# Performance work log

Measured on AMD Instinct MI355X. Metric: run time of the kernel, lower is better.

The kernel has to match this reference:

```python
import jax, jax.numpy as jnp
import numpy as np

BN_EPS = 1e-5


def _sparse(x, idx, W, b):
    # x: [B, N], idx: [N, K] int, W: [N, K], b: [N]
    # out[b, j] = sum_k x[b, idx[j, k]] * W[j, k] + b[j]
    g = jnp.take(x, idx, axis=1)            # [B, N, K]
    return jnp.einsum('bjk,jk->bj', g, W) + b


def _bn_train(x, gamma, beta):
    # BatchNorm1d in training mode: batch stats, biased variance
    m = jnp.mean(x, axis=0)
    v = jnp.mean(jnp.square(x - m), axis=0)
    return gamma * (x - m) * jax.lax.rsqrt(v + BN_EPS) + beta


def setup_inputs() -> dict:
    key = jax.random.key(0)
    ks = jax.random.split(key, 12)
    B, N = 16384, 784
    s = 0.5  # modest weight scale to keep the deep reuse-chain numerically tame
    return {
        'x':    jax.random.normal(ks[0], (B, N), dtype=jnp.float32),
        'idx1': jax.random.randint(ks[1], (N, 2), 0, N, dtype=jnp.int32),
        'W1':   jax.random.normal(ks[2], (N, 2), dtype=jnp.float32) * s,
        'b1':   jax.random.normal(ks[3], (N,), dtype=jnp.float32) * 0.1,
        'idx2': jax.random.randint(ks[4], (N, 4), 0, N, dtype=jnp.int32),
        'W2':   jax.random.normal(ks[5], (N, 4), dtype=jnp.float32) * s,
        'b2':   jax.random.normal(ks[6], (N,), dtype=jnp.float32) * 0.1,
        'idx3': jax.random.randint(ks[7], (N, 8), 0, N, dtype=jnp.int32),
        'W3':   jax.random.normal(ks[8], (N, 8), dtype=jnp.float32) * s,
        'b3':   jax.random.normal(ks[9], (N,), dtype=jnp.float32) * 0.1,
        'g2':   jnp.ones((N,), dtype=jnp.float32),
        'be2':  jnp.zeros((N,), dtype=jnp.float32),
        'g3':   jnp.ones((N,), dtype=jnp.float32),
        'be3':  jnp.zeros((N,), dtype=jnp.float32),
    }


def reference(x, idx1, W1, b1, idx2, W2, b2, idx3, W3, b3, g2, be2, g3, be3):
    gelu = lambda h: jax.nn.gelu(h, approximate=False)  # torch nn.GELU default (exact)
    h = gelu(_sparse(x, idx1, W1, b1))                  # sp1 -> gelu
    h = _bn_train(gelu(_sparse(h, idx2, W2, b2)), g2, be2)   # sp2 -> gelu -> bn2
    h = _bn_train(gelu(_sparse(h, idx3, W3, b3)), g3, be3)   # sp3 -> gelu -> bn3
    h = _bn_train(gelu(_sparse(h, idx2, W2, b2)), g2, be2)   # sp2 (reused) -> gelu -> bn2
    h = jax.nn.relu(_sparse(h, idx1, W1, b1))                # sp1 (reused) -> relu
    return h
```

## Files before the change

kernel.cpp:

```cpp
#include <hip/hip_runtime.h>
#include <math.h>

static constexpr int BROWS   = 16384;
static constexpr int NC      = 784;
static constexpr int TRB     = 16;
static constexpr int THREADS = 256;
static constexpr int NBLK    = BROWS / TRB;
static constexpr int NSLOT   = 4;
static constexpr int NREP    = 4;
static constexpr float EPS   = 1e-5f;
static constexpr float INV_B = 1.0f / (float)BROWS;

#if defined(__has_builtin)
#if __has_builtin(__builtin_amdgcn_global_load_lds)
#define HAVE_ASYNC_LDS 1
#endif
#if __has_builtin(__builtin_amdgcn_rcpf)
#define HAVE_RCPF 1
#endif
#if __has_builtin(__builtin_elementwise_fma)
#define HAVE_EW_FMA 1
#endif
#endif

typedef float v2f __attribute__((ext_vector_type(2)));

__device__ __forceinline__ void stage16(const float4* g, float4* l) {
#ifdef HAVE_ASYNC_LDS
    __builtin_amdgcn_global_load_lds(
        (const __attribute__((address_space(1))) void*)g,
        (__attribute__((address_space(3))) void*)l, 16, 0, 0);
#else
    *l = *g;
#endif
}

__device__ __forceinline__ unsigned short f2b(float f) {
    union { float f; unsigned u; } v; v.f = f;
    const unsigned r = v.u + 0x7fffu + ((v.u >> 16) & 1u);
    return (unsigned short)(r >> 16);
}
__device__ __forceinline__ unsigned pack2(float lo, float hi) {
    return (unsigned)f2b(lo) | ((unsigned)f2b(hi) << 16);
}
__device__ __forceinline__ unsigned long long pack4(float a, float b, float c, float d) {
    return (unsigned long long)pack2(a, b) | ((unsigned long long)pack2(c, d) << 32);
}
__device__ __forceinline__ float fast_rcp(float x) {
#ifdef HAVE_RCPF
    return __builtin_amdgcn_rcpf(x);
#else
    return 1.0f / x;
#endif
}

__device__ __forceinline__ float gelu_f(float x) {
    const float u  = x * x;
    const float z  = x * fmaf(0.0356774081f, u, 0.7978845608f);
    const float e  = __expf(2.0f * z);
    const float r  = fast_rcp(e + 1.0f);
    const float t  = fmaf(-2.0f, r, 1.0f);
    const float hx = 0.5f * x;
    return fmaf(hx, t, hx);
}

__device__ __forceinline__ void fmaq(const unsigned long long v, const float w, v2f acc[2]) {
    const unsigned lo = (unsigned)v, hi = (unsigned)(v >> 32);
    union { unsigned u; float f; } a0, a1, b0, b1;
    a0.u = lo << 16; a1.u = lo & 0xffff0000u;
    b0.u = hi << 16; b1.u = hi & 0xffff0000u;
    const v2f a = { a0.f, a1.f }, b = { b0.f, b1.f };
    const v2f w2 = { w, w };
#ifdef HAVE_EW_FMA
    acc[0] = __builtin_elementwise_fma(a, w2, acc[0]);
    acc[1] = __builtin_elementwise_fma(b, w2, acc[1]);
#else
    acc[0] += a * w2;
    acc[1] += b * w2;
#endif
}

template<int CH>
__device__ __forceinline__ void gchunk(const unsigned long long* __restrict__ tile,
                                       const int* ji, const float* jw,
                                       v2f acc[4][2])
{
    unsigned long long t[CH][4];
    #pragma unroll
    for (int k = 0; k < CH; ++k) {
        #pragma unroll
        for (int q = 0; q < 4; ++q) t[k][q] = tile[q * NC + ji[k]];
    }
    #pragma unroll
    for (int k = 0; k < CH; ++k) {
        #pragma unroll
        for (int q = 0; q < 4; ++q) fmaq(t[k][q], jw[k], acc[q]);
    }
}

template<int K>
__device__ __forceinline__ void gacc(const unsigned long long* __restrict__ tile,
                                     const int* ji, const float* jw, const float jb,
                                     v2f acc[4][2])
{
    #pragma unroll
    for (int q = 0; q < 4; ++q) { acc[q][0] = (v2f){ jb, jb }; acc[q][1] = (v2f){ jb, jb }; }
    if (K == 8) {
        gchunk<4>(tile, ji,     jw,     acc);
        gchunk<4>(tile, ji + 4, jw + 4, acc);
    } else {
        gchunk<K>(tile, ji, jw, acc);
    }
}

__global__ __launch_bounds__(THREADS, 5)
void k12(const float* __restrict__ x,
         const int* __restrict__ idx1, const float* __restrict__ W1, const float* __restrict__ b1,
         const int* __restrict__ idx2, const float* __restrict__ W2, const float* __restrict__ b2,
         unsigned long long* __restrict__ outr,
         float* __restrict__ ssum, float* __restrict__ ssq)
{
    __shared__ unsigned long long tile[4 * NC];
    const int tid  = threadIdx.x;
    const int row0 = blockIdx.x * TRB;

    #pragma unroll
    for (int s = 0; s < NSLOT; ++s) {
        const int c = tid + s * THREADS;
        if (c < NC) {
            #pragma unroll
            for (int q = 0; q < 4; ++q) {
                const size_t base = (size_t)(row0 + 4 * q) * NC + c;
                tile[q * NC + c] = pack4(x[base], x[base + NC], x[base + 2 * NC], x[base + 3 * NC]);
            }
        }
    }
    __syncthreads();

    unsigned long long o[NSLOT][4];
    #pragma unroll
    for (int s = 0; s < NSLOT; ++s) {
        const int j = tid + s * THREADS;
        if (j < NC) {
            int ji[2]; float jw[2];
            ji[0] = idx1[2 * j]; ji[1] = idx1[2 * j + 1];
            jw[0] = W1[2 * j];   jw[1] = W1[2 * j + 1];
            v2f acc[4][2];
            gacc<2>(tile, ji, jw, b1[j], acc);
            #pragma unroll
            for (int q = 0; q < 4; ++q)
                o[s][q] = pack4(gelu_f(acc[q][0].x), gelu_f(acc[q][0].y),
                                gelu_f(acc[q][1].x), gelu_f(acc[q][1].y));
        }
    }
    __syncthreads();
    #pragma unroll
    for (int s = 0; s < NSLOT; ++s) {
        const int j = tid + s * THREADS;
        if (j < NC) {
            #pragma unroll
            for (int q = 0; q < 4; ++q) tile[q * NC + j] = o[s][q];
        }
    }
    __syncthreads();

    const int rep = blockIdx.x & (NREP - 1);
    unsigned long long* dst = outr + (size_t)blockIdx.x * 4 * NC;
    #pragma unroll
    for (int s = 0; s < NSLOT; ++s) {
        const int j = tid + s * THREADS;
        if (j < NC) {
            int ji[4]; float jw[4];
            #pragma unroll
            for (int k = 0; k < 4; ++k) { ji[k] = idx2[4 * j + k]; jw[k] = W2[4 * j + k]; }
            v2f acc[4][2];
            gacc<4>(tile, ji, jw, b2[j], acc);
            float s1 = 0.0f, s2 = 0.0f;
            #pragma unroll
            for (int q = 0; q < 4; ++q) {
                const float u0 = gelu_f(acc[q][0].x), u1 = gelu_f(acc[q][0].y);
                const float u2 = gelu_f(acc[q][1].x), u3 = gelu_f(acc[q][1].y);
                s1 += (u0 + u1) + (u2 + u3);
                s2 = fmaf(u0, u0, fmaf(u1, u1, fmaf(u2, u2, fmaf(u3, u3, s2))));
                dst[q * NC + j] = pack4(u0, u1, u2, u3);
            }
            atomicAdd(&ssum[rep * NC + j], s1);
            atomicAdd(&ssq[rep * NC + j],  s2);
        }
    }
}

template<int K, bool FINAL>
__global__ __launch_bounds__(THREADS, 5)
void kbn(const unsigned long long* __restrict__ inr,
         const int* __restrict__ idx, const float* __restrict__ W, const float* __restrict__ bias,
         const float* __restrict__ gamma, const float* __restrict__ beta,
         const float* __restrict__ psum, const float* __restrict__ psq,
         unsigned long long* __restrict__ outr, float* __restrict__ fout,
         float* __restrict__ ssum, float* __restrict__ ssq)
{
    __shared__ unsigned long long tile[4 * NC];
    __shared__ float s_sc[NC], s_sh[NC];
    const int tid  = threadIdx.x;
    const int row0 = blockIdx.x * TRB;

    {
        const float4* src = (const float4*)(inr + (size_t)blockIdx.x * 4 * NC);
        float4*       dstl = (float4*)tile;
        for (int i = tid; i < 4 * NC / 2; i += THREADS) stage16(src + i, dstl + i);
    }
    for (int j = tid; j < NC; j += THREADS) {
        float s1 = 0.0f, s2 = 0.0f;
        #pragma unroll
        for (int r = 0; r < NREP; ++r) { s1 += psum[r * NC + j]; s2 += psq[r * NC + j]; }
        const float m   = s1 * INV_B;
        const float var = fmaf(-m, m, s2 * INV_B);
        const float sc  = gamma[j] * rsqrtf(var + EPS);
        s_sc[j] = sc;
        s_sh[j] = fmaf(-m, sc, beta[j]);
    }
    __syncthreads();

    const int rep = blockIdx.x & (NREP - 1);
    unsigned long long* dst = FINAL ? nullptr : (outr + (size_t)blockIdx.x * 4 * NC);
    #pragma unroll
    for (int s = 0; s < NSLOT; ++s) {
        const int j = tid + s * THREADS;
        if (j < NC) {
            int ji[K]; float jw[K];
            float jb = bias[j];
            #pragma unroll
            for (int k = 0; k < K; ++k) {
                const int   c = idx[K * j + k];
                const float w = W[K * j + k];
                ji[k] = c; jw[k] = w * s_sc[c]; jb = fmaf(w, s_sh[c], jb);
            }
            v2f acc[4][2];
            gacc<K>(tile, ji, jw, jb, acc);
            if (FINAL) {
                #pragma unroll
                for (int q = 0; q < 4; ++q) {
                    fout[(size_t)(row0 + 4 * q + 0) * NC + j] = fmaxf(acc[q][0].x, 0.0f);
                    fout[(size_t)(row0 + 4 * q + 1) * NC + j] = fmaxf(acc[q][0].y, 0.0f);
                    fout[(size_t)(row0 + 4 * q + 2) * NC + j] = fmaxf(acc[q][1].x, 0.0f);
                    fout[(size_t)(row0 + 4 * q + 3) * NC + j] = fmaxf(acc[q][1].y, 0.0f);
                }
            } else {
                float s1 = 0.0f, s2 = 0.0f;
                #pragma unroll
                for (int q = 0; q < 4; ++q) {
                    const float u0 = gelu_f(acc[q][0].x), u1 = gelu_f(acc[q][0].y);
                    const float u2 = gelu_f(acc[q][1].x), u3 = gelu_f(acc[q][1].y);
                    s1 += (u0 + u1) + (u2 + u3);
                    s2 = fmaf(u0, u0, fmaf(u1, u1, fmaf(u2, u2, fmaf(u3, u3, s2))));
                    dst[q * NC + j] = pack4(u0, u1, u2, u3);
                }
                atomicAdd(&ssum[rep * NC + j], s1);
                atomicAdd(&ssq[rep * NC + j],  s2);
            }
        }
    }
}

extern "C" void kernel_launch(void* const* d_in, const int* in_sizes, int n_in,
                              void* d_out, int out_size, void* d_ws, size_t ws_size,
                              hipStream_t stream)
{
    const float* x    = (const float*)d_in[0];
    const int*   idx1 = (const int*)  d_in[1];
    const float* W1   = (const float*)d_in[2];
    const float* b1   = (const float*)d_in[3];
    const int*   idx2 = (const int*)  d_in[4];
    const float* W2   = (const float*)d_in[5];
    const float* b2   = (const float*)d_in[6];
    const int*   idx3 = (const int*)  d_in[7];
    const float* W3   = (const float*)d_in[8];
    const float* b3   = (const float*)d_in[9];
    const float* g2   = (const float*)d_in[10];
    const float* be2  = (const float*)d_in[11];
    const float* g3   = (const float*)d_in[12];
    const float* be3  = (const float*)d_in[13];
    float* out = (float*)d_out;

    const size_t QN = (size_t)NBLK * 4 * NC;
    unsigned long long* r0 = (unsigned long long*)d_ws;
    unsigned long long* r1 = r0 + QN;
    float* p = (float*)(r1 + QN);
    float* sum2a = p; p += NREP * NC;  float* ssq2a = p; p += NREP * NC;
    float* sum3  = p; p += NREP * NC;  float* ssq3  = p; p += NREP * NC;
    float* sum2b = p; p += NREP * NC;  float* ssq2b = p; p += NREP * NC;

    hipMemsetAsync(sum2a, 0, 6 * NREP * NC * sizeof(float), stream);

    const dim3 grid(NBLK), blk(THREADS);

    k12<<<grid, blk, 0, stream>>>(x, idx1, W1, b1, idx2, W2, b2, r0, sum2a, ssq2a);
    kbn<8, false><<<grid, blk, 0, stream>>>(
        r0, idx3, W3, b3, g2, be2, sum2a, ssq2a, r1, nullptr, sum3, ssq3);
    kbn<4, false><<<grid, blk, 0, stream>>>(
        r1, idx2, W2, b2, g3, be3, sum3, ssq3, r0, nullptr, sum2b, ssq2b);
    kbn<2, true><<<grid, blk, 0, stream>>>(
        r0, idx1, W1, b1, g2, be2, sum2b, ssq2b, nullptr, out, nullptr, nullptr);
}
```

Measured before the change: 197.6 us.

## Fuse all sparse layers into one cooperative persistent kernel with grid barriers

Adds a cooperative kernel that keeps each block's 16-row tile in LDS across all five sparse layers. At each BatchNorm boundary it synchronises the whole grid with an arrive counter: the last block to arrive reduces the batch statistics and publishes the scale and shift, and the other blocks spin on a flag. This removes the bf16 intermediate round trips through global memory and three extra kernel launches. In exchange it needs every block resident at once, at 4 blocks per CU, and adds three grid-wide barriers, each with one block doing the reduction alone. The fallback multi-kernel path is retuned to 512 threads with split LDS tiles.

New measurement: 628.6 us. +218.1%, slower.

```diff
diff --git a/kernel.cpp b/kernel.cpp
--- a/kernel.cpp
+++ b/kernel.cpp
@@ -4,12 +4,15 @@
 static constexpr int BROWS   = 16384;
 static constexpr int NC      = 784;
 static constexpr int TRB     = 16;
-static constexpr int THREADS = 256;
 static constexpr int NBLK    = BROWS / TRB;
-static constexpr int NSLOT   = 4;
 static constexpr int NREP    = 4;
 static constexpr float EPS   = 1e-5f;
 static constexpr float INV_B = 1.0f / (float)BROWS;
+
+static constexpr int PTHREADS = 256;
+static constexpr int PNSLOT   = 4;
+static constexpr int FTHREADS = 512;
+static constexpr int FNSLOT   = 2;
 
 #if defined(__has_builtin)
 #if __has_builtin(__builtin_amdgcn_global_load_lds)
@@ -45,6 +48,12 @@
 }
 __device__ __forceinline__ unsigned long long pack4(float a, float b, float c, float d) {
     return (unsigned long long)pack2(a, b) | ((unsigned long long)pack2(c, d) << 32);
+}
+__device__ __forceinline__ unsigned long long pack_f2(float a, float b) {
+    union { float f[2]; unsigned long long u; } v; v.f[0] = a; v.f[1] = b; return v.u;
+}
+__device__ __forceinline__ void unpack_f2(unsigned long long u, float& a, float& b) {
+    union { float f[2]; unsigned long long u; } v; v.u = u; a = v.f[0]; b = v.f[1];
 }
 __device__ __forceinline__ float fast_rcp(float x) {
 #ifdef HAVE_RCPF
@@ -113,119 +122,22 @@
     }
 }
 
-__global__ __launch_bounds__(THREADS, 5)
-void k12(const float* __restrict__ x,
-         const int* __restrict__ idx1, const float* __restrict__ W1, const float* __restrict__ b1,
-         const int* __restrict__ idx2, const float* __restrict__ W2, const float* __restrict__ b2,
-         unsigned long long* __restrict__ outr,
-         float* __restrict__ ssum, float* __restrict__ ssq)
-{
-    __shared__ unsigned long long tile[4 * NC];
-    const int tid  = threadIdx.x;
-    const int row0 = blockIdx.x * TRB;
-
-    #pragma unroll
-    for (int s = 0; s < NSLOT; ++s) {
-        const int c = tid + s * THREADS;
-        if (c < NC) {
-            #pragma unroll
-            for (int q = 0; q < 4; ++q) {
-                const size_t base = (size_t)(row0 + 4 * q) * NC + c;
-                tile[q * NC + c] = pack4(x[base], x[base + NC], x[base + 2 * NC], x[base + 3 * NC]);
-            }
-        }
-    }
-    __syncthreads();
-
-    unsigned long long o[NSLOT][4];
-    #pragma unroll
-    for (int s = 0; s < NSLOT; ++s) {
-        const int j = tid + s * THREADS;
-        if (j < NC) {
-            int ji[2]; float jw[2];
-            ji[0] = idx1[2 * j]; ji[1] = idx1[2 * j + 1];
-            jw[0] = W1[2 * j];   jw[1] = W1[2 * j + 1];
-            v2f acc[4][2];
-            gacc<2>(tile, ji, jw, b1[j], acc);
-            #pragma unroll
-            for (int q = 0; q < 4; ++q)
-                o[s][q] = pack4(gelu_f(acc[q][0].x), gelu_f(acc[q][0].y),
-                                gelu_f(acc[q][1].x), gelu_f(acc[q][1].y));
-        }
-    }
-    __syncthreads();
-    #pragma unroll
-    for (int s = 0; s < NSLOT; ++s) {
-        const int j = tid + s * THREADS;
-        if (j < NC) {
-            #pragma unroll
-            for (int q = 0; q < 4; ++q) tile[q * NC + j] = o[s][q];
-        }
-    }
-    __syncthreads();
-
-    const int rep = blockIdx.x & (NREP - 1);
-    unsigned long long* dst = outr + (size_t)blockIdx.x * 4 * NC;
-    #pragma unroll
-    for (int s = 0; s < NSLOT; ++s) {
-        const int j = tid + s * THREADS;
-        if (j < NC) {
-            int ji[4]; float jw[4];
-            #pragma unroll
-            for (int k = 0; k < 4; ++k) { ji[k] = idx2[4 * j + k]; jw[k] = W2[4 * j + k]; }
-            v2f acc[4][2];
-            gacc<4>(tile, ji, jw, b2[j], acc);
-            float s1 = 0.0f, s2 = 0.0f;
-            #pragma unroll
-            for (int q = 0; q < 4; ++q) {
-                const float u0 = gelu_f(acc[q][0].x), u1 = gelu_f(acc[q][0].y);
-                const float u2 = gelu_f(acc[q][1].x), u3 = gelu_f(acc[q][1].y);
-                s1 += (u0 + u1) + (u2 + u3);
-                s2 = fmaf(u0, u0, fmaf(u1, u1, fmaf(u2, u2, fmaf(u3, u3, s2))));
-                dst[q * NC + j] = pack4(u0, u1, u2, u3);
-            }
-            atomicAdd(&ssum[rep * NC + j], s1);
-            atomicAdd(&ssq[rep * NC + j],  s2);
-        }
-    }
-}
-
-template<int K, bool FINAL>
-__global__ __launch_bounds__(THREADS, 5)
-void kbn(const unsigned long long* __restrict__ inr,
-         const int* __restrict__ idx, const float* __restrict__ W, const float* __restrict__ bias,
-         const float* __restrict__ gamma, const float* __restrict__ beta,
-         const float* __restrict__ psum, const float* __restrict__ psq,
-         unsigned long long* __restrict__ outr, float* __restrict__ fout,
-         float* __restrict__ ssum, float* __restrict__ ssq)
-{
-    __shared__ unsigned long long tile[4 * NC];
-    __shared__ float s_sc[NC], s_sh[NC];
-    const int tid  = threadIdx.x;
-    const int row0 = blockIdx.x * TRB;
-
-    {
-        const float4* src = (const float4*)(inr + (size_t)blockIdx.x * 4 * NC);
-        float4*       dstl = (float4*)tile;
-        for (int i = tid; i < 4 * NC / 2; i += THREADS) stage16(src + i, dstl + i);
-    }
-    for (int j = tid; j < NC; j += THREADS) {
-        float s1 = 0.0f, s2 = 0.0f;
-        #pragma unroll
-        for (int r = 0; r < NREP; ++r) { s1 += psum[r * NC + j]; s2 += psq[r * NC + j]; }
-        const float m   = s1 * INV_B;
-        const float var = fmaf(-m, m, s2 * INV_B);
-        const float sc  = gamma[j] * rsqrtf(var + EPS);
-        s_sc[j] = sc;
-        s_sh[j] = fmaf(-m, sc, beta[j]);
-    }
-    __syncthreads();
-
-    const int rep = blockIdx.x & (NREP - 1);
-    unsigned long long* dst = FINAL ? nullptr : (outr + (size_t)blockIdx.x * 4 * NC);
-    #pragma unroll
-    for (int s = 0; s < NSLOT; ++s) {
-        const int j = tid + s * THREADS;
+
+template<int K, bool FOLD, bool STATS, bool FINAL>
+__device__ __forceinline__ void pphase(
+    unsigned long long* __restrict__ tile,
+    const float* __restrict__ s_sc, const float* __restrict__ s_sh,
+    const int* __restrict__ idx, const float* __restrict__ W,
+    const float* __restrict__ bias,
+    const int tid, const int row0, const int rep,
+    float* __restrict__ psum, float* __restrict__ psq,
+    float* __restrict__ fout)
+{
+    unsigned long long o[PNSLOT][4];
+    float st1[PNSLOT], st2[PNSLOT];
+    #pragma unroll
+    for (int s = 0; s < PNSLOT; ++s) {
+        const int j = tid + s * PTHREADS;
         if (j < NC) {
             int ji[K]; float jw[K];
             float jb = bias[j];
@@ -233,7 +145,9 @@
             for (int k = 0; k < K; ++k) {
                 const int   c = idx[K * j + k];
                 const float w = W[K * j + k];
-                ji[k] = c; jw[k] = w * s_sc[c]; jb = fmaf(w, s_sh[c], jb);
+                ji[k] = c;
+                if (FOLD) { jw[k] = w * s_sc[c]; jb = fmaf(w, s_sh[c], jb); }
+                else      { jw[k] = w; }
             }
             v2f acc[4][2];
             gacc<K>(tile, ji, jw, jb, acc);
@@ -251,10 +165,273 @@
                 for (int q = 0; q < 4; ++q) {
                     const float u0 = gelu_f(acc[q][0].x), u1 = gelu_f(acc[q][0].y);
                     const float u2 = gelu_f(acc[q][1].x), u3 = gelu_f(acc[q][1].y);
+                    if (STATS) {
+                        s1 += (u0 + u1) + (u2 + u3);
+                        s2 = fmaf(u0, u0, fmaf(u1, u1, fmaf(u2, u2, fmaf(u3, u3, s2))));
+                    }
+                    o[s][q] = pack4(u0, u1, u2, u3);
+                }
+                st1[s] = s1; st2[s] = s2;
+            }
+        }
+    }
+    if (FINAL) return;
+    __syncthreads();
+    #pragma unroll
+    for (int s = 0; s < PNSLOT; ++s) {
+        const int j = tid + s * PTHREADS;
+        if (j < NC) {
+            #pragma unroll
+            for (int q = 0; q < 4; ++q) tile[q * NC + j] = o[s][q];
+            if (STATS) {
+                atomicAdd(&psum[rep * NC + j], st1[s]);
+                atomicAdd(&psq [rep * NC + j], st2[s]);
+            }
+        }
+    }
+    __syncthreads();
+}
+
+__device__ __forceinline__ void bn_barrier(
+    const int tid, const int bno,
+    const float* __restrict__ psum, const float* __restrict__ psq,
+    const float* __restrict__ gamma, const float* __restrict__ beta,
+    unsigned long long* __restrict__ scshG,
+    unsigned* __restrict__ arrive, unsigned* __restrict__ flag,
+    float* __restrict__ s_sc, float* __restrict__ s_sh, int* __restrict__ s_last)
+{
+    if (tid == 0) {
+        __threadfence();
+        const unsigned t = __hip_atomic_fetch_add(&arrive[bno], 1u,
+                              __ATOMIC_ACQ_REL, __HIP_MEMORY_SCOPE_AGENT);
+        *s_last = (t == (unsigned)(NBLK - 1));
+    }
+    __syncthreads();
+    if (*s_last) {
+        for (int j = tid; j < NC; j += PTHREADS) {
+            float s1 = 0.0f, s2 = 0.0f;
+            #pragma unroll
+            for (int r = 0; r < NREP; ++r) {
+                s1 += __hip_atomic_load(&psum[r * NC + j], __ATOMIC_RELAXED, __HIP_MEMORY_SCOPE_AGENT);
+                s2 += __hip_atomic_load(&psq [r * NC + j], __ATOMIC_RELAXED, __HIP_MEMORY_SCOPE_AGENT);
+            }
+            const float m   = s1 * INV_B;
+            const float var = fmaf(-m, m, s2 * INV_B);
+            const float sc  = gamma[j] * rsqrtf(var + EPS);
+            const float sh  = fmaf(-m, sc, beta[j]);
+            __hip_atomic_store(&scshG[j], pack_f2(sc, sh),
+                               __ATOMIC_RELAXED, __HIP_MEMORY_SCOPE_AGENT);
+        }
+        __syncthreads();
+        if (tid == 0)
+            __hip_atomic_store(&flag[bno], 1u, __ATOMIC_RELEASE, __HIP_MEMORY_SCOPE_AGENT);
+    } else if (tid == 0) {
+        while (__hip_atomic_load(&flag[bno], __ATOMIC_ACQUIRE, __HIP_MEMORY_SCOPE_AGENT) == 0u)
+            __builtin_amdgcn_s_sleep(32);
+    }
+    __syncthreads();
+    for (int j = tid; j < NC; j += PTHREADS) {
+        float sc, sh;
+        unpack_f2(__hip_atomic_load(&scshG[j], __ATOMIC_RELAXED, __HIP_MEMORY_SCOPE_AGENT), sc, sh);
+        s_sc[j] = sc; s_sh[j] = sh;
+    }
+    __syncthreads();
+}
+
+__global__ __launch_bounds__(PTHREADS, 4)
+void fusedp(const float* __restrict__ x,
+            const int* __restrict__ idx1, const float* __restrict__ W1, const float* __restrict__ b1,
+            const int* __restrict__ idx2, const float* __restrict__ W2, const float* __restrict__ b2,
+            const int* __restrict__ idx3, const float* __restrict__ W3, const float* __restrict__ b3,
+            const float* __restrict__ g2, const float* __restrict__ be2,
+            const float* __restrict__ g3, const float* __restrict__ be3,
+            float* __restrict__ out,
+            float* __restrict__ stats,
+            unsigned long long* __restrict__ scsh,
+            unsigned* __restrict__ sync)
+{
+    __shared__ unsigned long long tile[4 * NC];
+    __shared__ float s_sc[NC], s_sh[NC];
+    __shared__ int s_last;
+    const int tid  = threadIdx.x;
+    const int row0 = blockIdx.x * TRB;
+    const int rep  = blockIdx.x & (NREP - 1);
+
+    float* psumA = stats;                 float* psqA = psumA + NREP * NC;
+    float* psumB = psqA  + NREP * NC;     float* psqB = psumB + NREP * NC;
+    float* psumC = psqB  + NREP * NC;     float* psqC = psumC + NREP * NC;
+    unsigned* arrive = sync;
+    unsigned* flag   = sync + 4;
+
+    #pragma unroll
+    for (int s = 0; s < PNSLOT; ++s) {
+        const int c = tid + s * PTHREADS;
+        if (c < NC) {
+            #pragma unroll
+            for (int q = 0; q < 4; ++q) {
+                const size_t base = (size_t)(row0 + 4 * q) * NC + c;
+                tile[q * NC + c] = pack4(x[base], x[base + NC], x[base + 2 * NC], x[base + 3 * NC]);
+            }
+        }
+    }
+    __syncthreads();
+
+    pphase<2, false, false, false>(tile, s_sc, s_sh, idx1, W1, b1, tid, row0, rep,
+                                   nullptr, nullptr, nullptr);
+    pphase<4, false, true, false>(tile, s_sc, s_sh, idx2, W2, b2, tid, row0, rep,
+                                  psumA, psqA, nullptr);
+    bn_barrier(tid, 0, psumA, psqA, g2, be2, scsh,           arrive, flag, s_sc, s_sh, &s_last);
+    pphase<8, true, true, false>(tile, s_sc, s_sh, idx3, W3, b3, tid, row0, rep,
+                                 psumB, psqB, nullptr);
+    bn_barrier(tid, 1, psumB, psqB, g3, be3, scsh + NC,      arrive, flag, s_sc, s_sh, &s_last);
+    pphase<4, true, true, false>(tile, s_sc, s_sh, idx2, W2, b2, tid, row0, rep,
+                                 psumC, psqC, nullptr);
+    bn_barrier(tid, 2, psumC, psqC, g2, be2, scsh + 2 * NC,  arrive, flag, s_sc, s_sh, &s_last);
+    pphase<2, true, false, true>(tile, s_sc, s_sh, idx1, W1, b1, tid, row0, rep,
+                                 nullptr, nullptr, out);
+}
+
+
+__device__ __forceinline__ void fmaq2(const unsigned long long v, const float w, v2f acc[2]) {
+    fmaq(v, w, acc);
+}
+
+__global__ __launch_bounds__(FTHREADS, 6)
+void k12(const float* __restrict__ x,
+         const int* __restrict__ idx1, const float* __restrict__ W1, const float* __restrict__ b1,
+         const int* __restrict__ idx2, const float* __restrict__ W2, const float* __restrict__ b2,
+         unsigned long long* __restrict__ outr,
+         float* __restrict__ ssum, float* __restrict__ ssq)
+{
+    __shared__ unsigned long long tileX[4 * NC];
+    __shared__ unsigned long long tileH[4 * NC];
+    const int tid  = threadIdx.x;
+    const int row0 = blockIdx.x * TRB;
+
+    #pragma unroll
+    for (int slot = 0; slot < FNSLOT; ++slot) {
+        const int c = tid + slot * FTHREADS;
+        if (c < NC) {
+            #pragma unroll
+            for (int q = 0; q < 4; ++q) {
+                const size_t base = (size_t)(row0 + 4 * q) * NC + c;
+                tileX[q * NC + c] = pack4(x[base], x[base + NC], x[base + 2 * NC], x[base + 3 * NC]);
+            }
+        }
+    }
+    __syncthreads();
+
+    #pragma unroll
+    for (int slot = 0; slot < FNSLOT; ++slot) {
+        const int j = tid + slot * FTHREADS;
+        if (j < NC) {
+            const int   c0 = idx1[2 * j], c1 = idx1[2 * j + 1];
+            const float w0 = W1[2 * j],   w1 = W1[2 * j + 1], bb = b1[j];
+            #pragma unroll
+            for (int q = 0; q < 4; ++q) {
+                v2f acc[2] = { { bb, bb }, { bb, bb } };
+                fmaq2(tileX[q * NC + c0], w0, acc);
+                fmaq2(tileX[q * NC + c1], w1, acc);
+                tileH[q * NC + j] = pack4(gelu_f(acc[0].x), gelu_f(acc[0].y),
+                                          gelu_f(acc[1].x), gelu_f(acc[1].y));
+            }
+        }
+    }
+    __syncthreads();
+
+    const int rep = blockIdx.x & (NREP - 1);
+    unsigned long long* dst = outr + (size_t)blockIdx.x * 4 * NC;
+    #pragma unroll
+    for (int slot = 0; slot < FNSLOT; ++slot) {
+        const int j = tid + slot * FTHREADS;
+        if (j < NC) {
+            int ji[4]; float jw[4];
+            #pragma unroll
+            for (int k = 0; k < 4; ++k) { ji[k] = idx2[4 * j + k]; jw[k] = W2[4 * j + k]; }
+            const float jb = b2[j];
+            float s1 = 0.0f, s2 = 0.0f;
+            #pragma unroll
+            for (int q = 0; q < 4; ++q) {
+                v2f acc[2] = { { jb, jb }, { jb, jb } };
+                #pragma unroll
+                for (int k = 0; k < 4; ++k) fmaq2(tileH[q * NC + ji[k]], jw[k], acc);
+                const float u0 = gelu_f(acc[0].x), u1 = gelu_f(acc[0].y);
+                const float u2 = gelu_f(acc[1].x), u3 = gelu_f(acc[1].y);
+                s1 += (u0 + u1) + (u2 + u3);
+                s2 = fmaf(u0, u0, fmaf(u1, u1, fmaf(u2, u2, fmaf(u3, u3, s2))));
+                dst[q * NC + j] = pack4(u0, u1, u2, u3);
+            }
+            atomicAdd(&ssum[rep * NC + j], s1);
+            atomicAdd(&ssq[rep * NC + j],  s2);
+        }
+    }
+}
+
+template<int K, bool FINAL>
+__global__ __launch_bounds__(FTHREADS, 8)
+void kbn(const unsigned long long* __restrict__ inr,
+         const int* __restrict__ idx, const float* __restrict__ W, const float* __restrict__ bias,
+         const float* __restrict__ gamma, const float* __restrict__ beta,
+         const float* __restrict__ psum, const float* __restrict__ psq,
+         unsigned long long* __restrict__ outr, float* __restrict__ fout,
+         float* __restrict__ ssum, float* __restrict__ ssq)
+{
+    __shared__ unsigned long long tile[4 * NC];
+    __shared__ float s_sc[NC], s_sh[NC];
+    const int tid  = threadIdx.x;
+    const int row0 = blockIdx.x * TRB;
+
+    {
+        const float4* src = (const float4*)(inr + (size_t)blockIdx.x * 4 * NC);
+        float4*       dstl = (float4*)tile;
+        for (int i = tid; i < 4 * NC / 2; i += FTHREADS) stage16(src + i, dstl + i);
+    }
+    for (int j = tid; j < NC; j += FTHREADS) {
+        float s1 = 0.0f, s2 = 0.0f;
+        #pragma unroll
+        for (int r = 0; r < NREP; ++r) { s1 += psum[r * NC + j]; s2 += psq[r * NC + j]; }
+        const float m   = s1 * INV_B;
+        const float var = fmaf(-m, m, s2 * INV_B);
+        const float sc  = gamma[j] * rsqrtf(var + EPS);
+        s_sc[j] = sc;
+        s_sh[j] = fmaf(-m, sc, beta[j]);
+    }
+    __syncthreads();
+
+    const int rep = blockIdx.x & (NREP - 1);
+    unsigned long long* dst = FINAL ? nullptr : (outr + (size_t)blockIdx.x * 4 * NC);
+    #pragma unroll
+    for (int slot = 0; slot < FNSLOT; ++slot) {
+        const int j = tid + slot * FTHREADS;
+        if (j < NC) {
+            int ji[K]; float jw[K];
+            float jb = bias[j];
+            #pragma unroll
+            for (int k = 0; k < K; ++k) {
+                const int   c = idx[K * j + k];
+                const float w = W[K * j + k];
+                ji[k] = c; jw[k] = w * s_sc[c]; jb = fmaf(w, s_sh[c], jb);
+            }
+            float s1 = 0.0f, s2 = 0.0f;
+            #pragma unroll
+            for (int q = 0; q < 4; ++q) {
+                v2f acc[2] = { { jb, jb }, { jb, jb } };
+                #pragma unroll
+                for (int k = 0; k < K; ++k) fmaq2(tile[q * NC + ji[k]], jw[k], acc);
+                if (FINAL) {
+                    fout[(size_t)(row0 + 4 * q + 0) * NC + j] = fmaxf(acc[0].x, 0.0f);
+                    fout[(size_t)(row0 + 4 * q + 1) * NC + j] = fmaxf(acc[0].y, 0.0f);
+                    fout[(size_t)(row0 + 4 * q + 2) * NC + j] = fmaxf(acc[1].x, 0.0f);
+                    fout[(size_t)(row0 + 4 * q + 3) * NC + j] = fmaxf(acc[1].y, 0.0f);
+                } else {
+                    const float u0 = gelu_f(acc[0].x), u1 = gelu_f(acc[0].y);
+                    const float u2 = gelu_f(acc[1].x), u3 = gelu_f(acc[1].y);
                     s1 += (u0 + u1) + (u2 + u3);
                     s2 = fmaf(u0, u0, fmaf(u1, u1, fmaf(u2, u2, fmaf(u3, u3, s2))));
                     dst[q * NC + j] = pack4(u0, u1, u2, u3);
                 }
+            }
+            if (!FINAL) {
                 atomicAdd(&ssum[rep * NC + j], s1);
                 atomicAdd(&ssq[rep * NC + j],  s2);
             }
@@ -285,15 +462,29 @@
     const size_t QN = (size_t)NBLK * 4 * NC;
     unsigned long long* r0 = (unsigned long long*)d_ws;
     unsigned long long* r1 = r0 + QN;
-    float* p = (float*)(r1 + QN);
-    float* sum2a = p; p += NREP * NC;  float* ssq2a = p; p += NREP * NC;
-    float* sum3  = p; p += NREP * NC;  float* ssq3  = p; p += NREP * NC;
-    float* sum2b = p; p += NREP * NC;  float* ssq2b = p; p += NREP * NC;
-
-    hipMemsetAsync(sum2a, 0, 6 * NREP * NC * sizeof(float), stream);
-
-    const dim3 grid(NBLK), blk(THREADS);
-
+    float* stats = (float*)(r1 + QN);
+    unsigned* syncw = (unsigned*)(stats + 6 * NREP * NC);
+    unsigned long long* scsh = (unsigned long long*)(syncw + 8);
+
+    hipMemsetAsync(stats, 0, 6 * NREP * NC * sizeof(float) + 8 * sizeof(unsigned), stream);
+
+    void* args[] = {
+        (void*)&x,
+        (void*)&idx1, (void*)&W1, (void*)&b1,
+        (void*)&idx2, (void*)&W2, (void*)&b2,
+        (void*)&idx3, (void*)&W3, (void*)&b3,
+        (void*)&g2, (void*)&be2, (void*)&g3, (void*)&be3,
+        (void*)&out, (void*)&stats, (void*)&scsh, (void*)&syncw
+    };
+    const hipError_t err = hipLaunchCooperativeKernel(
+        (const void*)fusedp, dim3(NBLK), dim3(PTHREADS), args, 0, stream);
+    if (err == hipSuccess) return;
+
+    float* sum2a = stats;              float* ssq2a = sum2a + NREP * NC;
+    float* sum3  = ssq2a + NREP * NC;  float* ssq3  = sum3  + NREP * NC;
+    float* sum2b = ssq3  + NREP * NC;  float* ssq2b = sum2b + NREP * NC;
+
+    const dim3 grid(NBLK), blk(FTHREADS);
     k12<<<grid, blk, 0, stream>>>(x, idx1, W1, b1, idx2, W2, b2, r0, sum2a, ssq2a);
     kbn<8, false><<<grid, blk, 0, stream>>>(
         r0, idx3, W3, b3, g2, be2, sum2a, ssq2a, r1, nullptr, sum3, ssq3);
```
